# Performance work log

Measured on AMD Instinct MI355X. Metric: run time of the kernel, lower is better.

Reference implementation:

```python
import jax, jax.numpy as jnp
import numpy as np

DIM = 1024
EXP = 4           # expansion_factor
NUM_EXPERTS = 4
BATCH, SEQ = 4, 4096


def setup_inputs() -> dict:
    key = jax.random.key(0)
    ks = jax.random.split(key, 6)
    x = jax.random.normal(ks[0], (BATCH, SEQ, DIM), dtype=jnp.float32)
    token_mask = jax.random.randint(ks[1], (BATCH, SEQ), 0, NUM_EXPERTS, dtype=jnp.int32)
    hid = DIM * EXP
    s1 = 1.0 / np.sqrt(DIM)
    s2 = 1.0 / np.sqrt(hid)
    # nn.Linear layout: weight [out_features, in_features]
    w1 = jax.random.uniform(ks[2], (hid, DIM), minval=-s1, maxval=s1, dtype=jnp.float32)
    b1 = jax.random.uniform(ks[3], (hid,), minval=-s1, maxval=s1, dtype=jnp.float32)
    w2 = jax.random.uniform(ks[4], (DIM, hid), minval=-s2, maxval=s2, dtype=jnp.float32)
    b2 = jax.random.uniform(ks[5], (DIM,), minval=-s2, maxval=s2, dtype=jnp.float32)
    return {"x": x, "w1": w1, "b1": b1, "w2": w2, "b2": b2, "token_mask": token_mask}


def _nested_ffn(x, w1, b1, w2, b2, token_mask):
    dim = x.shape[-1]            # in_features of proj1
    out_dim = w2.shape[0]        # out_features of proj2 (== dim)
    # Expert m uses the first D_m = width >> (E-1-m) features (matryoshka nesting).
    # Expand (proj1): truncating input features to D_m and doing a full GEMM is
    # exactly equivalent to zeroing features >= D_m, so we mask then do one GEMM.
    d_in = dim >> (NUM_EXPERTS - 1 - token_mask)             # [B,S]
    in_mask = jnp.arange(dim) < d_in[..., None]              # [B,S,dim]
    h = jnp.einsum('bsd,fd->bsf', jnp.where(in_mask, x, jnp.zeros((), x.dtype)), w1) + b1
    h = jax.nn.gelu(h, approximate=False)                    # torch nn.GELU() default = erf
    # Contract (proj2): expert m produces only the first D_m outputs (incl. bias),
    # padded with zeros -> compute full GEMM then mask outputs.
    d_out = out_dim >> (NUM_EXPERTS - 1 - token_mask)        # [B,S]
    out_mask = jnp.arange(out_dim) < d_out[..., None]        # [B,S,out_dim]
    y = jnp.einsum('bsf,df->bsd', h, w2) + b2
    return jnp.where(out_mask, y, jnp.zeros((), y.dtype))


def reference(x, w1, b1, w2, b2, token_mask):
    return _nested_ffn(x, w1, b1, w2, b2, token_mask)
```

## Files before the change

kernel.cpp:

```cpp
#include <hip/hip_runtime.h>
#include <hip/hip_bf16.h>


typedef __bf16 bf16x8 __attribute__((ext_vector_type(8)));
typedef float f32x4 __attribute__((ext_vector_type(4)));

#define M_TOK   16384
#define DIM     1024
#define HID     4096

#define META_T     31
#define META_BLK   64
#define META_MAP   192
#define META_RT    1280

__device__ inline unsigned short f2bf(float f) {
  unsigned int u = __float_as_uint(f);
  u += 0x7fffu + ((u >> 16) & 1u);
  return (unsigned short)(u >> 16);
}

__device__ inline float gelu_f(float v) {
  float z = fabsf(v) * 0.7071067811865475f;
  float t = __builtin_amdgcn_rcpf(fmaf(0.3275911f, z, 1.0f));
  float p = fmaf(t, 1.061405429f, -1.453152027f);
  p = fmaf(t, p, 1.421413741f);
  p = fmaf(t, p, -0.284496736f);
  p = fmaf(t, p, 0.254829592f);
  p = p * t;
  float E = __expf(-0.5f * v * v);
  float er = fmaf(-p, E, 1.0f);
  er = copysignf(er, v);
  return 0.5f * v * (1.0f + er);
}

__device__ inline void async_copy16(const void* g, void* s) {
  __builtin_amdgcn_global_load_lds(
      (const __attribute__((address_space(1))) unsigned int*)g,
      (__attribute__((address_space(3))) unsigned int*)s,
      16, 0, 0);
}

template<int LDK>
__device__ inline void stage_tile(const unsigned short* __restrict__ g,
                                  int row0, int k0, char* lds) {
  const char* gbase = (const char*)g;
  int tid = threadIdx.x;
#pragma unroll
  for (int i = 0; i < 4; ++i) {
    int q = i * 256 + tid;
    int r = q >> 3;
    int c = q & 7;
    int gc = c ^ (r & 7);
    const void* gp = gbase + ((size_t)(row0 + r) * LDK + (size_t)k0 + gc * 8) * 2;
    async_copy16(gp, lds + (size_t)q * 16);
  }
}

__global__ __launch_bounds__(1024) void sort_kernel(const int* __restrict__ tm,
                                                    int* __restrict__ meta) {
  __shared__ int cnt[1024][5];
  __shared__ int sbase[5];
  __shared__ int cb[128];
  __shared__ int pfx[129];
  int tid = threadIdx.x;

  int c0 = 0, c1 = 0, c2 = 0, c3 = 0;
  unsigned int epack = 0;
  int4 tv[4];
#pragma unroll
  for (int j = 0; j < 4; ++j)
    tv[j] = *(const int4*)(tm + tid * 16 + j * 4);
#pragma unroll
  for (int j = 0; j < 4; ++j) {
    int e;
    e = tv[j].x; epack |= (unsigned)e << (2 * (4 * j + 0)); c0 += (e == 0); c1 += (e == 1); c2 += (e == 2); c3 += (e == 3);
    e = tv[j].y; epack |= (unsigned)e << (2 * (4 * j + 1)); c0 += (e == 0); c1 += (e == 1); c2 += (e == 2); c3 += (e == 3);
    e = tv[j].z; epack |= (unsigned)e << (2 * (4 * j + 2)); c0 += (e == 0); c1 += (e == 1); c2 += (e == 2); c3 += (e == 3);
    e = tv[j].w; epack |= (unsigned)e << (2 * (4 * j + 3)); c0 += (e == 0); c1 += (e == 1); c2 += (e == 2); c3 += (e == 3);
  }
  cnt[tid][0] = c0; cnt[tid][1] = c1; cnt[tid][2] = c2; cnt[tid][3] = c3;
  __syncthreads();
  for (int s = 1; s < 1024; s <<= 1) {
    int v0 = 0, v1 = 0, v2 = 0, v3 = 0;
    if (tid >= s) {
      v0 = cnt[tid - s][0]; v1 = cnt[tid - s][1];
      v2 = cnt[tid - s][2]; v3 = cnt[tid - s][3];
    }
    __syncthreads();
    cnt[tid][0] += v0; cnt[tid][1] += v1; cnt[tid][2] += v2; cnt[tid][3] += v3;
    __syncthreads();
  }
  if (tid == 0) {
    int b = 0;
#pragma unroll
    for (int e = 0; e < 4; ++e) { sbase[e] = b; b += cnt[1023][e]; }
    sbase[4] = b;
  }
  __syncthreads();
  int off0 = sbase[0] + cnt[tid][0] - c0;
  int off1 = sbase[1] + cnt[tid][1] - c1;
  int off2 = sbase[2] + cnt[tid][2] - c2;
  int off3 = sbase[3] + cnt[tid][3] - c3;
  int* rowtok = meta + META_RT;
#pragma unroll
  for (int j = 0; j < 16; ++j) {
    int e = (epack >> (2 * j)) & 3;
    int t = tid * 16 + j;
    int pos = (e == 0) ? off0++ : (e == 1) ? off1++ : (e == 2) ? off2++ : off3++;
    rowtok[pos] = t | (e << 14);
  }
  if (tid < 128) {
    int last = tid * 128 + 127;
    int e = (last >= sbase[1]) + (last >= sbase[2]) + (last >= sbase[3]);
    meta[META_BLK + tid] = 128 << e;
    cb[tid] = 1 << e;
  }
  __syncthreads();
  if (tid == 0) {
    int acc = 0;
    for (int j = 0; j < 128; ++j) { pfx[j] = acc; acc += cb[j]; }
    pfx[128] = acc;
    meta[META_T] = acc;
  }
  __syncthreads();
  if (tid < 128) {
    int n = cb[tid];
    int p = pfx[tid];
    int* map = meta + META_MAP;
    for (int c = 0; c < n; ++c) map[p + c] = tid * 8 + c;
    int zp = pfx[128] + 8 * tid - pfx[tid];
    for (int c = n; c < 8; ++c) map[zp + (c - n)] = tid * 8 + c;
  }
}

__global__ void prep_kernel(const float* __restrict__ x,
                            const float* __restrict__ w1,
                            const float* __restrict__ w2,
                            const int* __restrict__ meta,
                            unsigned short* __restrict__ xb,
                            unsigned short* __restrict__ w1b,
                            unsigned short* __restrict__ w2b) {
  int b = blockIdx.x;
  int tid = threadIdx.x;
  if (b < M_TOK) {
    int mt = meta[META_RT + b];
    int t = mt & 0x3FFF;
    int din = 128 << (mt >> 14);
    int d = tid * 4;
    float4 v = *(const float4*)(x + (size_t)t * DIM + d);
    ushort4 o;
    if (d < din) {
      o.x = f2bf(v.x); o.y = f2bf(v.y); o.z = f2bf(v.z); o.w = f2bf(v.w);
    } else {
      o.x = 0; o.y = 0; o.z = 0; o.w = 0;
    }
    *(ushort4*)(xb + (size_t)b * DIM + d) = o;
  } else {
    size_t i = (size_t)(b - M_TOK) * 1024 + tid * 4;
    const float* src;
    unsigned short* dst;
    if (i < (size_t)HID * DIM) { src = w1; dst = w1b; }
    else { src = w2 - (size_t)HID * DIM; dst = w2b - (size_t)HID * DIM; }
    float4 v = *(const float4*)(src + i);
    ushort4 o;
    o.x = f2bf(v.x); o.y = f2bf(v.y); o.z = f2bf(v.z); o.w = f2bf(v.w);
    *(ushort4*)(dst + i) = o;
  }
}

__global__ __launch_bounds__(256) void gemm1_kernel(
    const unsigned short* __restrict__ A,
    const unsigned short* __restrict__ B,
    const float* __restrict__ bias,
    const int* __restrict__ meta,
    unsigned short* __restrict__ H)
{
  constexpr int K = DIM, N = HID;
  __shared__ char smem[32768];
  char* As = smem;
  char* Bs = smem + 16384;
  int tid = threadIdx.x;
  int lane = tid & 63, quad = lane >> 4, l15 = lane & 15;
  int wave = tid >> 6, wm = wave & 1, wn = wave >> 1;
  int row0 = blockIdx.x * 128, col0 = blockIdx.y * 128;
  int kmax = meta[META_BLK + blockIdx.x];

  int chb = (quad ^ (l15 & 7)) << 4;

  f32x4 acc[4][4] = {};

  for (int k0 = 0; k0 < kmax; k0 += 64) {
    __syncthreads();
    stage_tile<K>(A, row0, k0, As);
    stage_tile<K>(B, col0, k0, Bs);
    __syncthreads();
#pragma unroll
    for (int kk = 0; kk < 2; ++kk) {
      int xo = chb ^ (kk << 6);
      bf16x8 af[4], bg[4];
#pragma unroll
      for (int mt = 0; mt < 4; ++mt)
        af[mt] = *(const bf16x8*)(As + (wm * 64 + mt * 16 + l15) * 128 + xo);
#pragma unroll
      for (int nt = 0; nt < 4; ++nt)
        bg[nt] = *(const bf16x8*)(Bs + (wn * 64 + nt * 16 + l15) * 128 + xo);
#pragma unroll
      for (int mt = 0; mt < 4; ++mt)
#pragma unroll
        for (int nt = 0; nt < 4; ++nt)
          acc[mt][nt] = __builtin_amdgcn_mfma_f32_16x16x32_bf16(
              af[mt], bg[nt], acc[mt][nt], 0, 0, 0);
    }
  }

  __syncthreads();
  {
    int wb = (wm * 64 + quad * 4) * 256 + wn * 128 + (quad << 5) + l15 * 2;
#pragma unroll
    for (int nt = 0; nt < 4; ++nt) {
      int f = col0 + wn * 64 + nt * 16 + l15;
      float bv = bias[f];
      int xadr = wb ^ (nt << 5);
#pragma unroll
      for (int mt = 0; mt < 4; ++mt) {
#pragma unroll
        for (int r = 0; r < 4; ++r) {
          float v = gelu_f(acc[mt][nt][r] + bv);
          *(unsigned short*)(smem + xadr + mt * 4096 + r * 256) = f2bf(v);
        }
      }
    }
  }
  __syncthreads();
  {
    int row = tid >> 4;
    int c = tid & 15;
    int raddr = row * 256 + ((((c >> 1) ^ ((row >> 2) & 3))) << 5) + ((c & 1) << 4);
    const unsigned short* hbase = H;
    size_t gb = (size_t)(row0 + row) * N + col0 + c * 8;
#pragma unroll
    for (int i = 0; i < 8; ++i) {
      bf16x8 v = *(const bf16x8*)(smem + raddr + i * 4096);
      *(bf16x8*)(hbase + gb + (size_t)i * 16 * N) = v;
    }
  }
}

__global__ __launch_bounds__(256) void gemm2_kernel(
    const unsigned short* __restrict__ A,
    const unsigned short* __restrict__ B,
    const float* __restrict__ bias,
    const int* __restrict__ meta,
    float* __restrict__ out)
{
  constexpr int K = HID, N = DIM;
  int T = meta[META_T];
  int b = blockIdx.x;
  int mp = meta[META_MAP + b];
  int row0 = (mp >> 3) * 128, col0 = (mp & 7) * 128;
  const int* rowtok = meta + META_RT;
  int tid = threadIdx.x;

  if (b >= T) {
    float4 z = make_float4(0.f, 0.f, 0.f, 0.f);
#pragma unroll
    for (int i = 0; i < 16; ++i) {
      int idx = i * 256 + tid;
      int r = idx >> 5;
      int col = (idx & 31) * 4;
      int t = rowtok[row0 + r] & 0x3FFF;
      *(float4*)(out + (size_t)t * N + col0 + col) = z;
    }
    return;
  }

  __shared__ char smem[32768];
  char* As = smem;
  char* Bs = smem + 16384;
  int lane = tid & 63, quad = lane >> 4, l15 = lane & 15;
  int wave = tid >> 6, wm = wave & 1, wn = wave >> 1;
  int chb = (quad ^ (l15 & 7)) << 4;

  f32x4 acc[4][4] = {};

  for (int k0 = 0; k0 < K; k0 += 64) {
    __syncthreads();
    stage_tile<K>(A, row0, k0, As);
    stage_tile<K>(B, col0, k0, Bs);
    __syncthreads();
#pragma unroll
    for (int kk = 0; kk < 2; ++kk) {
      int xo = chb ^ (kk << 6);
      bf16x8 af[4], bg[4];
#pragma unroll
      for (int mt = 0; mt < 4; ++mt)
        af[mt] = *(const bf16x8*)(As + (wm * 64 + mt * 16 + l15) * 128 + xo);
#pragma unroll
      for (int nt = 0; nt < 4; ++nt)
        bg[nt] = *(const bf16x8*)(Bs + (wn * 64 + nt * 16 + l15) * 128 + xo);
#pragma unroll
      for (int mt = 0; mt < 4; ++mt)
#pragma unroll
        for (int nt = 0; nt < 4; ++nt)
          acc[mt][nt] = __builtin_amdgcn_mfma_f32_16x16x32_bf16(
              af[mt], bg[nt], acc[mt][nt], 0, 0, 0);
    }
  }

  int p_base = row0 + wm * 64;
  int d_base = col0 + wn * 64;
#pragma unroll
  for (int mt = 0; mt < 4; ++mt) {
#pragma unroll
    for (int r = 0; r < 4; ++r) {
      int m2 = rowtok[p_base + mt * 16 + quad * 4 + r];
      int t = m2 & 0x3FFF;
      int dout = 128 << (m2 >> 14);
#pragma unroll
      for (int nt = 0; nt < 4; ++nt) {
        int d = d_base + nt * 16 + l15;
        float v = acc[mt][nt][r] + bias[d];
        out[(size_t)t * N + d] = (d < dout) ? v : 0.0f;
      }
    }
  }
}

extern "C" void kernel_launch(void* const* d_in, const int* in_sizes, int n_in,
                              void* d_out, int out_size, void* d_ws, size_t ws_size,
                              hipStream_t stream) {
  const float* x  = (const float*)d_in[0];
  const float* w1 = (const float*)d_in[1];
  const float* b1 = (const float*)d_in[2];
  const float* w2 = (const float*)d_in[3];
  const float* b2 = (const float*)d_in[4];
  const int*   tm = (const int*)d_in[5];
  float* out = (float*)d_out;

  char* ws = (char*)d_ws;
  int* meta = (int*)ws;
  unsigned short* xb  = (unsigned short*)(ws + 131072);
  unsigned short* w1b = (unsigned short*)(ws + 33685504);
  unsigned short* w2b = (unsigned short*)(ws + 42074112);
  unsigned short* hb  = (unsigned short*)(ws + 50462720);

  sort_kernel<<<1, 1024, 0, stream>>>(tm, meta);
  prep_kernel<<<M_TOK + 8192, 256, 0, stream>>>(x, w1, w2, meta, xb, w1b, w2b);
  gemm1_kernel<<<dim3(M_TOK / 128, HID / 128), 256, 0, stream>>>(xb, w1b, b1, meta, hb);
  gemm2_kernel<<<1024, 256, 0, stream>>>(hb, w2b, b2, meta, out);
}
```

Measured before the change: 371.0 us.

## Halve gemm2 row tiles, reorder gemm1 blocks heavy-first, drop LDS epilogue

The row-tile map in the sort kernel is rebuilt at 64-row granularity so gemm2 can use 64x128 tiles. This doubles the number of blocks and gives finer-grained skipping of zeroed output columns per expert group. gemm1 now uses a 1D grid that visits the heaviest (largest-K) row blocks first to balance load. Its epilogue writes GELU outputs straight to global memory instead of staging them through LDS. The direct writes are scattered 2-byte stores, which are much less coalesced than the previous 16-byte staged stores.

```diff
diff --git a/kernel.cpp b/kernel.cpp
--- a/kernel.cpp
+++ b/kernel.cpp
@@ -11,8 +11,8 @@
 
 #define META_T     31
 #define META_BLK   64
-#define META_MAP   192
-#define META_RT    1280
+#define META_MAP   256
+#define META_RT    2560
 
 __device__ inline unsigned short f2bf(float f) {
   unsigned int u = __float_as_uint(f);
@@ -41,13 +41,13 @@
       16, 0, 0);
 }
 
-template<int LDK>
+template<int ROWS, int LDK>
 __device__ inline void stage_tile(const unsigned short* __restrict__ g,
                                   int row0, int k0, char* lds) {
   const char* gbase = (const char*)g;
   int tid = threadIdx.x;
 #pragma unroll
-  for (int i = 0; i < 4; ++i) {
+  for (int i = 0; i < ROWS / 32; ++i) {
     int q = i * 256 + tid;
     int r = q >> 3;
     int c = q & 7;
@@ -61,8 +61,8 @@
                                                     int* __restrict__ meta) {
   __shared__ int cnt[1024][5];
   __shared__ int sbase[5];
-  __shared__ int cb[128];
-  __shared__ int pfx[129];
+  __shared__ int cb[256];
+  __shared__ int pfx[257];
   int tid = threadIdx.x;
 
   int c0 = 0, c1 = 0, c2 = 0, c3 = 0;
@@ -110,26 +110,26 @@
     int pos = (e == 0) ? off0++ : (e == 1) ? off1++ : (e == 2) ? off2++ : off3++;
     rowtok[pos] = t | (e << 14);
   }
-  if (tid < 128) {
-    int last = tid * 128 + 127;
+  if (tid < 256) {
+    int last = tid * 64 + 63;
     int e = (last >= sbase[1]) + (last >= sbase[2]) + (last >= sbase[3]);
-    meta[META_BLK + tid] = 128 << e;
     cb[tid] = 1 << e;
+    if (tid & 1) meta[META_BLK + (tid >> 1)] = 128 << e;
   }
   __syncthreads();
   if (tid == 0) {
     int acc = 0;
-    for (int j = 0; j < 128; ++j) { pfx[j] = acc; acc += cb[j]; }
-    pfx[128] = acc;
+    for (int j = 0; j < 256; ++j) { pfx[j] = acc; acc += cb[j]; }
+    pfx[256] = acc;
     meta[META_T] = acc;
   }
   __syncthreads();
-  if (tid < 128) {
+  if (tid < 256) {
     int n = cb[tid];
     int p = pfx[tid];
     int* map = meta + META_MAP;
     for (int c = 0; c < n; ++c) map[p + c] = tid * 8 + c;
-    int zp = pfx[128] + 8 * tid - pfx[tid];
+    int zp = pfx[256] + 8 * tid - pfx[tid];
     for (int c = n; c < 8; ++c) map[zp + (c - n)] = tid * 8 + c;
   }
 }
@@ -183,8 +183,9 @@
   int tid = threadIdx.x;
   int lane = tid & 63, quad = lane >> 4, l15 = lane & 15;
   int wave = tid >> 6, wm = wave & 1, wn = wave >> 1;
-  int row0 = blockIdx.x * 128, col0 = blockIdx.y * 128;
-  int kmax = meta[META_BLK + blockIdx.x];
+  int rowblk = 127 - (blockIdx.x >> 5);
+  int row0 = rowblk * 128, col0 = (blockIdx.x & 31) * 128;
+  int kmax = meta[META_BLK + rowblk];
 
   int chb = (quad ^ (l15 & 7)) << 4;
 
@@ -192,8 +193,8 @@
 
   for (int k0 = 0; k0 < kmax; k0 += 64) {
     __syncthreads();
-    stage_tile<K>(A, row0, k0, As);
-    stage_tile<K>(B, col0, k0, Bs);
+    stage_tile<128, K>(A, row0, k0, As);
+    stage_tile<128, K>(B, col0, k0, Bs);
     __syncthreads();
 #pragma unroll
     for (int kk = 0; kk < 2; ++kk) {
@@ -214,35 +215,20 @@
     }
   }
 
-  __syncthreads();
-  {
-    int wb = (wm * 64 + quad * 4) * 256 + wn * 128 + (quad << 5) + l15 * 2;
-#pragma unroll
-    for (int nt = 0; nt < 4; ++nt) {
-      int f = col0 + wn * 64 + nt * 16 + l15;
-      float bv = bias[f];
-      int xadr = wb ^ (nt << 5);
-#pragma unroll
-      for (int mt = 0; mt < 4; ++mt) {
-#pragma unroll
-        for (int r = 0; r < 4; ++r) {
-          float v = gelu_f(acc[mt][nt][r] + bv);
-          *(unsigned short*)(smem + xadr + mt * 4096 + r * 256) = f2bf(v);
-        }
+  int t_base = row0 + wm * 64;
+  int f_base = col0 + wn * 64;
+#pragma unroll
+  for (int nt = 0; nt < 4; ++nt) {
+    int f = f_base + nt * 16 + l15;
+    float bv = bias[f];
+#pragma unroll
+    for (int mt = 0; mt < 4; ++mt) {
+#pragma unroll
+      for (int r = 0; r < 4; ++r) {
+        int t = t_base + mt * 16 + quad * 4 + r;
+        float v = gelu_f(acc[mt][nt][r] + bv);
+        H[(size_t)t * N + f] = f2bf(v);
       }
-    }
-  }
-  __syncthreads();
-  {
-    int row = tid >> 4;
-    int c = tid & 15;
-    int raddr = row * 256 + ((((c >> 1) ^ ((row >> 2) & 3))) << 5) + ((c & 1) << 4);
-    const unsigned short* hbase = H;
-    size_t gb = (size_t)(row0 + row) * N + col0 + c * 8;
-#pragma unroll
-    for (int i = 0; i < 8; ++i) {
-      bf16x8 v = *(const bf16x8*)(smem + raddr + i * 4096);
-      *(bf16x8*)(hbase + gb + (size_t)i * 16 * N) = v;
     }
   }
 }
@@ -258,14 +244,14 @@
   int T = meta[META_T];
   int b = blockIdx.x;
   int mp = meta[META_MAP + b];
-  int row0 = (mp >> 3) * 128, col0 = (mp & 7) * 128;
+  int row0 = (mp >> 3) * 64, col0 = (mp & 7) * 128;
   const int* rowtok = meta + META_RT;
   int tid = threadIdx.x;
 
   if (b >= T) {
     float4 z = make_float4(0.f, 0.f, 0.f, 0.f);
 #pragma unroll
-    for (int i = 0; i < 16; ++i) {
+    for (int i = 0; i < 8; ++i) {
       int idx = i * 256 + tid;
       int r = idx >> 5;
       int col = (idx & 31) * 4;
@@ -275,32 +261,32 @@
     return;
   }
 
-  __shared__ char smem[32768];
+  __shared__ char smem[24576];
   char* As = smem;
-  char* Bs = smem + 16384;
+  char* Bs = smem + 8192;
   int lane = tid & 63, quad = lane >> 4, l15 = lane & 15;
   int wave = tid >> 6, wm = wave & 1, wn = wave >> 1;
   int chb = (quad ^ (l15 & 7)) << 4;
 
-  f32x4 acc[4][4] = {};
+  f32x4 acc[2][4] = {};
 
   for (int k0 = 0; k0 < K; k0 += 64) {
     __syncthreads();
-    stage_tile<K>(A, row0, k0, As);
-    stage_tile<K>(B, col0, k0, Bs);
+    stage_tile<64, K>(A, row0, k0, As);
+    stage_tile<128, K>(B, col0, k0, Bs);
     __syncthreads();
 #pragma unroll
     for (int kk = 0; kk < 2; ++kk) {
       int xo = chb ^ (kk << 6);
-      bf16x8 af[4], bg[4];
-#pragma unroll
-      for (int mt = 0; mt < 4; ++mt)
-        af[mt] = *(const bf16x8*)(As + (wm * 64 + mt * 16 + l15) * 128 + xo);
+      bf16x8 af[2], bg[4];
+#pragma unroll
+      for (int mt = 0; mt < 2; ++mt)
+        af[mt] = *(const bf16x8*)(As + (wm * 32 + mt * 16 + l15) * 128 + xo);
 #pragma unroll
       for (int nt = 0; nt < 4; ++nt)
         bg[nt] = *(const bf16x8*)(Bs + (wn * 64 + nt * 16 + l15) * 128 + xo);
 #pragma unroll
-      for (int mt = 0; mt < 4; ++mt)
+      for (int mt = 0; mt < 2; ++mt)
 #pragma unroll
         for (int nt = 0; nt < 4; ++nt)
           acc[mt][nt] = __builtin_amdgcn_mfma_f32_16x16x32_bf16(
@@ -308,10 +294,10 @@
     }
   }
 
-  int p_base = row0 + wm * 64;
+  int p_base = row0 + wm * 32;
   int d_base = col0 + wn * 64;
 #pragma unroll
-  for (int mt = 0; mt < 4; ++mt) {
+  for (int mt = 0; mt < 2; ++mt) {
 #pragma unroll
     for (int r = 0; r < 4; ++r) {
       int m2 = rowtok[p_base + mt * 16 + quad * 4 + r];
@@ -347,6 +333,6 @@
 
   sort_kernel<<<1, 1024, 0, stream>>>(tm, meta);
   prep_kernel<<<M_TOK + 8192, 256, 0, stream>>>(x, w1, w2, meta, xb, w1b, w2b);
-  gemm1_kernel<<<dim3(M_TOK / 128, HID / 128), 256, 0, stream>>>(xb, w1b, b1, meta, hb);
-  gemm2_kernel<<<1024, 256, 0, stream>>>(hb, w2b, b2, meta, out);
-}
+  gemm1_kernel<<<4096, 256, 0, stream>>>(xb, w1b, b1, meta, hb);
+  gemm2_kernel<<<2048, 256, 0, stream>>>(hb, w2b, b2, meta, out);
+}
```

Result: no change. 363.7 us (-2.0%).
